# Kernel tuning notes

Measured on AMD Instinct MI355X. Metric: run time of the kernel, lower is better.

Reference implementation:

```python
import jax, jax.numpy as jnp
import numpy as np


def _gather_tree(step_ids, parent_ids, max_seq_lens, end_token):
    """Vectorized beam-search backtrace.

    step_ids, parent_ids: [max_len, batch, beam] int32
    max_seq_lens: [batch] int32
    Returns beams: [max_len, batch, beam]
    """
    max_len, batch, beam = step_ids.shape
    # current back-pointer per (batch, beam); starts at own beam index
    own = jnp.broadcast_to(jnp.arange(beam, dtype=step_ids.dtype), (batch, beam))
    msl = jnp.minimum(max_seq_lens, max_len)[:, None]  # [batch, 1]

    def step(cur, xs):
        t, s_t, p_t = xs  # s_t, p_t: [batch, beam]
        active = t < msl  # [batch, 1] -> broadcasts over beam
        tok = jnp.where(active, jnp.take_along_axis(s_t, cur, axis=1), end_token)
        new_cur = jnp.where(active, jnp.take_along_axis(p_t, cur, axis=1), cur)
        return new_cur, tok

    ts = jnp.arange(max_len - 1, -1, -1, dtype=msl.dtype)
    _, toks = jax.lax.scan(step, own, (ts, step_ids[::-1], parent_ids[::-1]))
    beams = toks[::-1]  # [max_len, batch, beam]
    # once an end_token is produced, every later position becomes end_token
    ended = jnp.cumsum((beams == end_token).astype(jnp.int32), axis=0) > 0
    return jnp.where(ended, jnp.asarray(end_token, beams.dtype), beams)


def setup_inputs() -> dict:
    key = jax.random.key(0)
    k1, k2, k3 = jax.random.split(key, 3)
    max_len, batch, beam = 256, 4096, 8
    output_ids = jax.random.randint(k1, (max_len, batch, beam), 0, 32000, dtype=jnp.int32)
    parent_ids = jax.random.randint(k2, (max_len, batch, beam), 0, beam, dtype=jnp.int32)
    out_seq_lens = jax.random.randint(k3, (batch, beam), 0, max_len, dtype=jnp.int32)
    return {
        "output_ids": output_ids,
        "parent_ids": parent_ids,
        "out_seq_lens": out_seq_lens,
        "end_id": 2,
    }


def reference(output_ids, parent_ids, out_seq_lens, end_id):
    # finalize(): per-batch max decode length over beams
    max_lens = jnp.max(out_seq_lens, axis=1)  # [batch]
    ids = _gather_tree(output_ids, parent_ids, max_lens, end_id)  # [max_len, batch, beam]
    ids = jnp.transpose(ids, (1, 2, 0))  # einsum 'ijk->jki' -> [batch, beam, max_len]
    lengths = jnp.sum((ids != end_id).astype(output_ids.dtype), axis=-1)  # [batch, beam]
    return ids, lengths
```

## Files before the change

kernel.cpp:

```cpp
#include <hip/hip_runtime.h>


constexpr int MAX_LEN = 256;
constexpr int BATCH   = 4096;
constexpr int BEAM    = 8;
constexpr int NCHAIN  = BATCH * BEAM;
constexpr int PITCH   = 65;
constexpr unsigned ID_MAP = 0xFAC688u;

__global__ __launch_bounds__(256)
void gather_tree_kernel(const int* __restrict__ step_ids,
                        const int* __restrict__ parent_ids,
                        const int* __restrict__ seq_lens,
                        const int* __restrict__ end_id_p,
                        int* __restrict__ out_ids,
                        int* __restrict__ out_lens)
{
    __shared__ int      s_tile[MAX_LEN * PITCH];
    __shared__ unsigned hist[4 * 8 * 64];
    __shared__ unsigned segmap[4 * 8];
    __shared__ int      fe_buf[4 * 64];

    const int tid   = threadIdx.x;
    const int w     = tid >> 6;
    const int lane  = tid & 63;
    const int b_loc = lane >> 3;
    const int h     = lane & 7;
    const int bj0   = blockIdx.x * 64;
    const int tbase = w * 64;
    const int end_tok = *end_id_p;

    int sl = seq_lens[bj0 + lane];
    sl = max(sl, __shfl_xor(sl, 1));
    sl = max(sl, __shfl_xor(sl, 2));
    sl = max(sl, __shfl_xor(sl, 4));
    const int msl = min(sl, MAX_LEN);

    int cur = h;
    for (int kb = 56; kb >= 0; kb -= 8) {
        unsigned hw = 0;
        #pragma unroll
        for (int i = 7; i >= 0; --i) {
            const int t = tbase + kb + i;
            const int gidx = t * NCHAIN + bj0 + lane;
            int s = step_ids[gidx];
            int p = parent_ids[gidx];
            s_tile[t * PITCH + lane] = s;
            unsigned m = (unsigned)(p & 7) << (3 * h);
            m |= (unsigned)__shfl_xor((int)m, 1);
            m |= (unsigned)__shfl_xor((int)m, 2);
            m |= (unsigned)__shfl_xor((int)m, 4);
            const unsigned me = (t < msl) ? m : ID_MAP;
            hw |= (unsigned)cur << (3 * i);
            cur = (me >> (3 * cur)) & 7;
        }
        hist[(w * 8 + (kb >> 3)) * 64 + lane] = hw;
    }
    unsigned fm = (unsigned)cur << (3 * h);
    fm |= (unsigned)__shfl_xor((int)fm, 1);
    fm |= (unsigned)__shfl_xor((int)fm, 2);
    fm |= (unsigned)__shfl_xor((int)fm, 4);
    if (h == 0) segmap[w * 8 + b_loc] = fm;

    __syncthreads();

    int e = h;
    for (int ww = 3; ww > w; --ww)
        e = (segmap[ww * 8 + b_loc] >> (3 * e)) & 7;

    int fe = MAX_LEN;
    for (int kb = 0; kb < 64; kb += 8) {
        const unsigned hw = hist[(w * 8 + (kb >> 3)) * 64 + b_loc * 8 + e];
        #pragma unroll
        for (int i = 0; i < 8; ++i) {
            const int t = tbase + kb + i;
            const int c = (hw >> (3 * i)) & 7;
            int tok = s_tile[t * PITCH + b_loc * 8 + c];
            tok = (t < msl) ? tok : end_tok;
            if (tok == end_tok) fe = min(fe, t);
            s_tile[t * PITCH + lane] = tok;
        }
    }
    fe_buf[w * 64 + lane] = fe;

    __syncthreads();

    const int feg = min(min(fe_buf[lane], fe_buf[64 + lane]),
                        min(fe_buf[128 + lane], fe_buf[192 + lane]));
    if (w == 0) out_lens[bj0 + lane] = feg;

    const int t = tbase + lane;
    for (int c0 = 0; c0 < 64; ++c0) {
        const int fec = __shfl(feg, c0);
        const int v = s_tile[t * PITCH + c0];
        out_ids[(bj0 + c0) * MAX_LEN + t] = (t < fec) ? v : end_tok;
    }
}

extern "C" void kernel_launch(void* const* d_in, const int* in_sizes, int n_in,
                              void* d_out, int out_size, void* d_ws, size_t ws_size,
                              hipStream_t stream)
{
    const int* step_ids   = (const int*)d_in[0];
    const int* parent_ids = (const int*)d_in[1];
    const int* seq_lens   = (const int*)d_in[2];
    const int* end_id     = (const int*)d_in[3];

    int* out_ids  = (int*)d_out;
    int* out_lens = (int*)d_out + MAX_LEN * NCHAIN;

    gather_tree_kernel<<<NCHAIN / 64, 256, 0, stream>>>(
        step_ids, parent_ids, seq_lens, end_id, out_ids, out_lens);
}
```

Before: 109.6 us.

## Split time axis across 16 wavefronts and gather parents via shuffle

Each block now runs 16 wavefronts (1024 threads), with each wave covering a 16-step time segment instead of 64, so the serial backtrace per wave is shorter. The per-step parent lookup becomes a single indexed shuffle instead of building a packed map with three xor-shuffles. The transposed output store is reorganised so each wave writes 4 chains along contiguous time, which gives coalesced rows. The cross-segment composition loop grows to up to 15 steps, and 1024-thread blocks with about 66KB of LDS may limit occupancy.

```diff
diff --git a/kernel.cpp b/kernel.cpp
--- a/kernel.cpp
+++ b/kernel.cpp
@@ -6,9 +6,10 @@
 constexpr int BEAM    = 8;
 constexpr int NCHAIN  = BATCH * BEAM;
 constexpr int PITCH   = 65;
-constexpr unsigned ID_MAP = 0xFAC688u;
+constexpr int NW      = 16;
+constexpr int SEG     = 16;
 
-__global__ __launch_bounds__(256)
+__global__ __launch_bounds__(1024)
 void gather_tree_kernel(const int* __restrict__ step_ids,
                         const int* __restrict__ parent_ids,
                         const int* __restrict__ seq_lens,
@@ -17,9 +18,9 @@
                         int* __restrict__ out_lens)
 {
     __shared__ int      s_tile[MAX_LEN * PITCH];
-    __shared__ unsigned hist[4 * 8 * 64];
-    __shared__ unsigned segmap[4 * 8];
-    __shared__ int      fe_buf[4 * 64];
+    __shared__ unsigned hist[NW * 2 * 64];
+    __shared__ unsigned segmap[NW * 8];
+    __shared__ int      fe_buf[NW * 64];
 
     const int tid   = threadIdx.x;
     const int w     = tid >> 6;
@@ -27,7 +28,7 @@
     const int b_loc = lane >> 3;
     const int h     = lane & 7;
     const int bj0   = blockIdx.x * 64;
-    const int tbase = w * 64;
+    const int tbase = w * SEG;
     const int end_tok = *end_id_p;
 
     int sl = seq_lens[bj0 + lane];
@@ -37,24 +38,20 @@
     const int msl = min(sl, MAX_LEN);
 
     int cur = h;
-    for (int kb = 56; kb >= 0; kb -= 8) {
+    for (int kb = SEG - 8; kb >= 0; kb -= 8) {
         unsigned hw = 0;
         #pragma unroll
         for (int i = 7; i >= 0; --i) {
             const int t = tbase + kb + i;
-            const int gidx = t * NCHAIN + bj0 + lane;
-            int s = step_ids[gidx];
-            int p = parent_ids[gidx];
+            const int g = t * NCHAIN + bj0 + lane;
+            int s = step_ids[g];
+            int p = parent_ids[g];
             s_tile[t * PITCH + lane] = s;
-            unsigned m = (unsigned)(p & 7) << (3 * h);
-            m |= (unsigned)__shfl_xor((int)m, 1);
-            m |= (unsigned)__shfl_xor((int)m, 2);
-            m |= (unsigned)__shfl_xor((int)m, 4);
-            const unsigned me = (t < msl) ? m : ID_MAP;
+            int pg = __shfl(p, b_loc * 8 + cur);
             hw |= (unsigned)cur << (3 * i);
-            cur = (me >> (3 * cur)) & 7;
+            cur = (t < msl) ? (pg & 7) : cur;
         }
-        hist[(w * 8 + (kb >> 3)) * 64 + lane] = hw;
+        hist[(w * 2 + (kb >> 3)) * 64 + lane] = hw;
     }
     unsigned fm = (unsigned)cur << (3 * h);
     fm |= (unsigned)__shfl_xor((int)fm, 1);
@@ -65,12 +62,12 @@
     __syncthreads();
 
     int e = h;
-    for (int ww = 3; ww > w; --ww)
+    for (int ww = NW - 1; ww > w; --ww)
         e = (segmap[ww * 8 + b_loc] >> (3 * e)) & 7;
 
     int fe = MAX_LEN;
-    for (int kb = 0; kb < 64; kb += 8) {
-        const unsigned hw = hist[(w * 8 + (kb >> 3)) * 64 + b_loc * 8 + e];
+    for (int kb = 0; kb < SEG; kb += 8) {
+        const unsigned hw = hist[(w * 2 + (kb >> 3)) * 64 + b_loc * 8 + e];
         #pragma unroll
         for (int i = 0; i < 8; ++i) {
             const int t = tbase + kb + i;
@@ -85,15 +82,21 @@
 
     __syncthreads();
 
-    const int feg = min(min(fe_buf[lane], fe_buf[64 + lane]),
-                        min(fe_buf[128 + lane], fe_buf[192 + lane]));
+    int feg = fe_buf[lane];
+    #pragma unroll
+    for (int w2 = 1; w2 < NW; ++w2) feg = min(feg, fe_buf[w2 * 64 + lane]);
     if (w == 0) out_lens[bj0 + lane] = feg;
 
-    const int t = tbase + lane;
-    for (int c0 = 0; c0 < 64; ++c0) {
-        const int fec = __shfl(feg, c0);
-        const int v = s_tile[t * PITCH + c0];
-        out_ids[(bj0 + c0) * MAX_LEN + t] = (t < fec) ? v : end_tok;
+    #pragma unroll
+    for (int cc = 0; cc < 4; ++cc) {
+        const int c = w * 4 + cc;
+        const int fec = __shfl(feg, c);
+        #pragma unroll
+        for (int k = 0; k < 4; ++k) {
+            const int t = k * 64 + lane;
+            const int v = s_tile[t * PITCH + c];
+            out_ids[(bj0 + c) * MAX_LEN + t] = (t < fec) ? v : end_tok;
+        }
     }
 }
 
@@ -109,6 +112,6 @@
     int* out_ids  = (int*)d_out;
     int* out_lens = (int*)d_out + MAX_LEN * NCHAIN;
 
-    gather_tree_kernel<<<NCHAIN / 64, 256, 0, stream>>>(
+    gather_tree_kernel<<<NCHAIN / 64, 1024, 0, stream>>>(
         step_ids, parent_ids, seq_lens, end_id, out_ids, out_lens);
 }
```

New measurement: 105.1 us. 4.1% less time.
